# Optimization experiments

Measured on AMD Instinct MI355X. Metric: run time of the kernel, lower is better.

The kernel has to match this reference:

```python
import jax, jax.numpy as jnp
import numpy as np

B, N, DIM = 4, 4096, 1024
HEADS, DIM_HEAD, M = 16, 64, 128
DIM_INNER = HEADS * DIM_HEAD
SCALE = DIM_HEAD ** -0.5


def setup_inputs() -> dict:
    key = jax.random.key(0)
    ks = jax.random.split(key, 7)
    x = jax.random.normal(ks[0], (B, N, DIM), dtype=jnp.float32)
    mask = jax.random.bernoulli(ks[1], 0.9, (B, N))  # bool [b, n]
    W_qkv = jax.random.normal(ks[2], (DIM, 3 * DIM_INNER), dtype=jnp.float32) * (DIM ** -0.5)
    agent_tokens = jax.random.normal(ks[3], (HEADS, M, DIM_HEAD), dtype=jnp.float32) * 0.02
    W_qa = jax.random.normal(ks[4], (HEADS, HEADS), dtype=jnp.float32) * (HEADS ** -0.5)
    W_ak = jax.random.normal(ks[5], (HEADS, HEADS), dtype=jnp.float32) * (HEADS ** -0.5)
    W_out = jax.random.normal(ks[6], (DIM_INNER, DIM), dtype=jnp.float32) * (DIM_INNER ** -0.5)
    return {"x": x, "mask": mask, "W_qkv": W_qkv, "agent_tokens": agent_tokens,
            "W_qa": W_qa, "W_ak": W_ak, "W_out": W_out}


def reference(x, mask, W_qkv, agent_tokens, W_qa, W_ak, W_out):
    b, n, _ = x.shape
    h, m, d = agent_tokens.shape
    # qkv projection -> [3, b, h, n, d]  (layout matches 'b n (qkv h d)')
    qkv = (x @ W_qkv).reshape(b, n, 3, h, d).transpose(2, 0, 3, 1, 4)
    q, k, v = qkv[0], qkv[1], qkv[2]
    a = agent_tokens * SCALE  # [h, m, d]
    # stage 1: query-agent similarities [b, h, n, m]
    qa_sim = jnp.einsum('bhid,hjd->bhij', q, a)
    # stage 2: agent-key similarities [b, h, m, n]
    ak_sim = jnp.einsum('hid,bhjd->bhij', a, k)
    max_neg = -jnp.finfo(ak_sim.dtype).max
    ak_sim = jnp.where(mask[:, None, None, :], ak_sim, max_neg)
    qa_attn = jax.nn.softmax(qa_sim, axis=-1)
    ak_attn = jax.nn.softmax(ak_sim, axis=-1)
    # talking heads: 1x1 conv over head dim == head-mixing matmul
    qa_attn = jnp.einsum('gh,bhij->bgij', W_qa, qa_attn)
    ak_attn = jnp.einsum('gh,bhij->bgij', W_ak, ak_attn)
    agent_out = jnp.einsum('bhmn,bhnd->bhmd', ak_attn, v)    # [b, h, m, d]
    out = jnp.einsum('bhnm,bhmd->bhnd', qa_attn, agent_out)  # [b, h, n, d]
    out = jnp.where(mask[:, None, :, None], out, 0.0)
    out = out.transpose(0, 2, 1, 3).reshape(b, n, h * d)
    return out @ W_out
```

## Files before the change

kernel.cpp:

```cpp
#include <hip/hip_runtime.h>
#include <stdint.h>

#define DEVI __device__ __forceinline__

typedef __bf16 bf16x8 __attribute__((ext_vector_type(8)));
typedef float  f32x4  __attribute__((ext_vector_type(4)));
typedef unsigned int u32x2 __attribute__((ext_vector_type(2)));


DEVI unsigned short f2bf(float f) {
  union { float f; unsigned int u; } c; c.f = f;
  return (unsigned short)((c.u + 0x7fffu + ((c.u >> 16) & 1u)) >> 16);
}
DEVI float bf2f(unsigned short s) {
  union { unsigned int u; float f; } c; c.u = ((unsigned int)s) << 16;
  return c.f;
}
DEVI u32x2 pack4(float a, float b, float c, float d) {
  u32x2 r;
  r.x = (unsigned)f2bf(a) | ((unsigned)f2bf(b) << 16);
  r.y = (unsigned)f2bf(c) | ((unsigned)f2bf(d) << 16);
  return r;
}
DEVI bf16x8 ldg8(const unsigned short* p) { return *(const bf16x8*)p; }

DEVI void g2l16(const void* g, void* l) {
  __builtin_amdgcn_global_load_lds(
      (const __attribute__((address_space(1))) unsigned int*)g,
      (__attribute__((address_space(3))) unsigned int*)l, 16, 0, 0);
}

#define MFMA16(acc, a, b) acc = __builtin_amdgcn_mfma_f32_16x16x32_bf16((a), (b), (acc), 0, 0, 0)

#define VMCNT8() asm volatile("s_waitcnt vmcnt(8)")
#define VMCNT4() asm volatile("s_waitcnt vmcnt(4)")
#define VMCNT0() asm volatile("s_waitcnt vmcnt(0)")
#define LGKM0()  asm volatile("s_waitcnt lgkmcnt(0)")
#define SBAR()   __builtin_amdgcn_s_barrier()

__global__ __launch_bounds__(256) void k_prep(
    const float* __restrict__ x, const float* __restrict__ Wqkv,
    const float* __restrict__ ag, const float* __restrict__ Wout,
    unsigned short* __restrict__ Xb, unsigned short* __restrict__ WqkvT,
    unsigned short* __restrict__ Ab, unsigned short* __restrict__ WoT,
    float* __restrict__ rowsum)
{
  __shared__ float ldsT[32][33];
  const int tid = threadIdx.x;
  int bx = blockIdx.x;
  if (bx < 16384) {
    size_t i4 = ((size_t)bx * 256 + tid) * 4;
    f32x4 v = *(const f32x4*)&x[i4];
    *(u32x2*)&Xb[i4] = pack4(v[0], v[1], v[2], v[3]);
    return;
  }
  bx -= 16384;
  if (bx < 3072) {
    int jt = bx % 96, kt = bx / 96;
    int r32 = tid >> 3, c4 = (tid & 7) * 4;
    f32x4 v = *(const f32x4*)&Wqkv[(size_t)(kt * 32 + r32) * 3072 + jt * 32 + c4];
#pragma unroll
    for (int i = 0; i < 4; i++) ldsT[r32][c4 + i] = v[i];
    __syncthreads();
    float o0 = ldsT[c4 + 0][r32], o1 = ldsT[c4 + 1][r32];
    float o2 = ldsT[c4 + 2][r32], o3 = ldsT[c4 + 3][r32];
    *(u32x2*)&WqkvT[(size_t)(jt * 32 + r32) * 1024 + kt * 32 + c4] = pack4(o0, o1, o2, o3);
    return;
  }
  bx -= 3072;
  if (bx < 128) {
    size_t i4 = ((size_t)bx * 256 + tid) * 4;
    f32x4 v = *(const f32x4*)&ag[i4];
    *(u32x2*)&Ab[i4] = pack4(v[0] * 0.125f, v[1] * 0.125f, v[2] * 0.125f, v[3] * 0.125f);
    return;
  }
  bx -= 128;
  if (bx < 1024) {
    int ct = bx % 32, dt = bx / 32;
    int r32 = tid >> 3, c4 = (tid & 7) * 4;
    f32x4 v = *(const f32x4*)&Wout[(size_t)(dt * 32 + r32) * 1024 + ct * 32 + c4];
#pragma unroll
    for (int i = 0; i < 4; i++) ldsT[r32][c4 + i] = v[i];
    __syncthreads();
    float o0 = ldsT[c4 + 0][r32], o1 = ldsT[c4 + 1][r32];
    float o2 = ldsT[c4 + 2][r32], o3 = ldsT[c4 + 3][r32];
    *(u32x2*)&WoT[(size_t)(ct * 32 + r32) * 1024 + dt * 32 + c4] = pack4(o0, o1, o2, o3);
    return;
  }
  bx -= 1024;
  {
    const f32x4 z = {0.f, 0.f, 0.f, 0.f};
    *(f32x4*)&rowsum[((size_t)bx * 256 + tid) * 4] = z;
  }
}

DEVI void gemm_core_256(const unsigned short* __restrict__ A,
                        const unsigned short* __restrict__ Bt,
                        int row0, int col0, int swap,
                        unsigned short (*lds)[16384], f32x4 acc[8][4])
{
  const int tid = threadIdx.x, lane = tid & 63, w = tid >> 6;
  const int q = lane >> 4, r = lane & 15;
  const int wm = w >> 2, wn = w & 3;
  const int loff = r * 32 + ((q ^ ((r >> 1) & 3)) << 3);
  const int wslot = w * 512;
  const int scol = ((tid & 3) ^ ((tid >> 3) & 3)) << 3;
  const int srow = tid >> 2;
  const unsigned short* gA0 = A + (size_t)(row0 + srow) * 1024 + scol;
  const unsigned short* gA1 = gA0 + (size_t)128 * 1024;
  const unsigned short* gB0 = Bt + (size_t)(col0 + srow) * 1024 + scol;
  const unsigned short* gB1 = gB0 + (size_t)128 * 1024;
  const int aoff = (swap ? 8192 : 0) + wm * 4096;
  const int boff = (swap ? 0 : 8192) + wn * 2048;

  const f32x4 z = {0.f, 0.f, 0.f, 0.f};
#pragma unroll
  for (int i = 0; i < 8; i++)
#pragma unroll
    for (int j = 0; j < 4; j++) acc[i][j] = z;

#pragma unroll
  for (int pt = 0; pt < 3; ++pt) {
    unsigned short* lr = &lds[pt][0] + wslot;
    g2l16(gA0 + pt * 32, lr);
    g2l16(gA1 + pt * 32, lr + 4096);
    g2l16(gB0 + pt * 32, lr + 8192);
    g2l16(gB1 + pt * 32, lr + 12288);
  }
  VMCNT8();
  SBAR();

  for (int t = 0; t < 32; ++t) {
    const unsigned short* rp = &lds[t & 3][0];
    const unsigned short* pA = rp + aoff + loff;
    const unsigned short* pB = rp + boff + loff;
    bf16x8 af[4], bv[4];
#pragma unroll
    for (int rt = 0; rt < 4; rt++) af[rt] = *(const bf16x8*)(pA + rt * 512);
#pragma unroll
    for (int ct = 0; ct < 4; ct++) bv[ct] = *(const bf16x8*)(pB + ct * 512);
    if (t < 29) {
      unsigned short* lr = &lds[(t + 3) & 3][0] + wslot;
      size_t ko = (size_t)(t + 3) * 32;
      g2l16(gA0 + ko, lr);
      g2l16(gA1 + ko, lr + 4096);
    }
    SBAR();
    LGKM0();
    __builtin_amdgcn_s_setprio(1);
#pragma unroll
    for (int rt = 0; rt < 4; rt++)
#pragma unroll
      for (int ct = 0; ct < 4; ct++) MFMA16(acc[rt][ct], af[rt], bv[ct]);
    __builtin_amdgcn_s_setprio(0);
    SBAR();
#pragma unroll
    for (int rt = 0; rt < 4; rt++) af[rt] = *(const bf16x8*)(pA + (rt + 4) * 512);
    if (t < 29) {
      unsigned short* lr = &lds[(t + 3) & 3][0] + wslot;
      size_t ko = (size_t)(t + 3) * 32;
      g2l16(gB0 + ko, lr + 8192);
      g2l16(gB1 + ko, lr + 12288);
    }
    if (t < 29)      { VMCNT8(); }
    else if (t == 29) { VMCNT4(); }
    else if (t == 30) { VMCNT0(); }
    SBAR();
    LGKM0();
    __builtin_amdgcn_s_setprio(1);
#pragma unroll
    for (int rt = 0; rt < 4; rt++)
#pragma unroll
      for (int ct = 0; ct < 4; ct++) MFMA16(acc[rt + 4][ct], af[rt], bv[ct]);
    __builtin_amdgcn_s_setprio(0);
    SBAR();
  }
}

__global__ __launch_bounds__(512, 2) void k_gemm_qkv(
    const unsigned short* __restrict__ A, const unsigned short* __restrict__ Bt,
    unsigned short* __restrict__ Q, unsigned short* __restrict__ Kd,
    unsigned short* __restrict__ Vt)
{
  __shared__ __align__(16) unsigned short lds[4][16384];
  const int tid = threadIdx.x, lane = tid & 63, w = tid >> 6;
  const int q = lane >> 4, r = lane & 15, wm = w >> 2, wn = w & 3;
  const int row0 = blockIdx.x * 256, col0 = blockIdx.y * 256;
  const bool qk = blockIdx.y < 8;

  f32x4 acc[8][4];
  gemm_core_256(A, Bt, row0, col0, qk ? 1 : 0, lds, acc);

  const int b = row0 >> 12, row0b = row0 & 4095;
  if (qk) {
    unsigned short* dst = (col0 < 1024) ? Q : Kd;
    const int jb = (col0 & 1023) + wm * 128;
#pragma unroll
    for (int rt = 0; rt < 8; rt++)
#pragma unroll
      for (int ct = 0; ct < 4; ct++) {
        int j = jb + rt * 16 + 4 * q;
        int h = j >> 6, d0 = j & 63;
        int n = row0b + wn * 64 + ct * 16 + r;
        u32x2 pk = pack4(acc[rt][ct][0], acc[rt][ct][1], acc[rt][ct][2], acc[rt][ct][3]);
        *(u32x2*)&dst[(((size_t)(b * 16 + h)) * 4096 + n) * 64 + d0] = pk;
      }
  } else {
    const int jb = (col0 - 2048) + wn * 64;
#pragma unroll
    for (int rt = 0; rt < 8; rt++)
#pragma unroll
      for (int ct = 0; ct < 4; ct++) {
        int j = jb + ct * 16 + r;
        int h = j >> 6, d = j & 63;
        int n = row0b + wm * 128 + rt * 16 + 4 * q;
        u32x2 pk = pack4(acc[rt][ct][0], acc[rt][ct][1], acc[rt][ct][2], acc[rt][ct][3]);
        *(u32x2*)&Vt[(((size_t)(b * 16 + h)) * 64 + d) * 4096 + n] = pk;
      }
  }
}

__global__ __launch_bounds__(256, 2) void k_qk(
    const unsigned short* __restrict__ Q, const unsigned short* __restrict__ Kd,
    const unsigned short* __restrict__ Ab, const int* __restrict__ mask,
    unsigned short* __restrict__ QA, unsigned short* __restrict__ E,
    float* __restrict__ rowsum)
{
  const int tid = threadIdx.x, lane = tid & 63, w = tid >> 6;
  const int q = lane >> 4, r = lane & 15, wr = w >> 1, wc = w & 1;
  const int nt = blockIdx.x, h = blockIdx.y, b = blockIdx.z;
  const unsigned short* Qb = Q + (((size_t)(b * 16 + h)) * 4096 + nt * 128) * 64;
  const unsigned short* Kb = Kd + (((size_t)(b * 16 + h)) * 4096 + nt * 128) * 64;
  const unsigned short* Ah = Ab + (size_t)h * 8192;
  __shared__ float rs[2][128];
  const f32x4 z = {0.f, 0.f, 0.f, 0.f};

  {
    f32x4 acc[4][4];
#pragma unroll
    for (int i = 0; i < 4; i++)
#pragma unroll
      for (int j = 0; j < 4; j++) acc[i][j] = z;
#pragma unroll
    for (int ks = 0; ks < 2; ks++) {
      bf16x8 af[4], bv[4];
#pragma unroll
      for (int rt = 0; rt < 4; rt++) af[rt] = ldg8(Ah + (size_t)(64 * wr + 16 * rt + r) * 64 + ks * 32 + q * 8);
#pragma unroll
      for (int ct = 0; ct < 4; ct++) bv[ct] = ldg8(Qb + (size_t)(64 * wc + 16 * ct + r) * 64 + ks * 32 + q * 8);
#pragma unroll
      for (int rt = 0; rt < 4; rt++)
#pragma unroll
        for (int ct = 0; ct < 4; ct++) MFMA16(acc[rt][ct], af[rt], bv[ct]);
    }
    float cs[4];
#pragma unroll
    for (int ct = 0; ct < 4; ct++) {
      float s = 0.f;
#pragma unroll
      for (int rt = 0; rt < 4; rt++)
#pragma unroll
        for (int reg = 0; reg < 4; reg++) {
          float e = __expf(acc[rt][ct][reg]);
          acc[rt][ct][reg] = e; s += e;
        }
      s += __shfl_xor(s, 16); s += __shfl_xor(s, 32);
      cs[ct] = s;
    }
    if (q == 0) {
#pragma unroll
      for (int ct = 0; ct < 4; ct++) rs[wr][64 * wc + 16 * ct + r] = cs[ct];
    }
    __syncthreads();
#pragma unroll
    for (int ct = 0; ct < 4; ct++) {
      int nl = 64 * wc + 16 * ct + r;
      float inv = 1.0f / (rs[0][nl] + rs[1][nl]);
      int n = nt * 128 + nl;
      size_t base = (((size_t)(b * 16 + h)) * 4096 + n) * 128;
#pragma unroll
      for (int rt = 0; rt < 4; rt++) {
        int m0 = 64 * wr + 16 * rt + 4 * q;
        u32x2 pk = pack4(acc[rt][ct][0] * inv, acc[rt][ct][1] * inv,
                         acc[rt][ct][2] * inv, acc[rt][ct][3] * inv);
        *(u32x2*)&QA[base + m0] = pk;
      }
    }
  }
  __syncthreads();

  {
    f32x4 acc[4][4];
#pragma unroll
    for (int i = 0; i < 4; i++)
#pragma unroll
      for (int j = 0; j < 4; j++) acc[i][j] = z;
#pragma unroll
    for (int ks = 0; ks < 2; ks++) {
      bf16x8 af[4], bv[4];
#pragma unroll
      for (int rt = 0; rt < 4; rt++) af[rt] = ldg8(Kb + (size_t)(64 * wr + 16 * rt + r) * 64 + ks * 32 + q * 8);
#pragma unroll
      for (int ct = 0; ct < 4; ct++) bv[ct] = ldg8(Ah + (size_t)(64 * wc + 16 * ct + r) * 64 + ks * 32 + q * 8);
#pragma unroll
      for (int rt = 0; rt < 4; rt++)
#pragma unroll
        for (int ct = 0; ct < 4; ct++) MFMA16(acc[rt][ct], af[rt], bv[ct]);
    }
    float cs[4] = {0.f, 0.f, 0.f, 0.f};
#pragma unroll
    for (int rt = 0; rt < 4; rt++) {
      const int4 mkv = *(const int4*)&mask[b * 4096 + nt * 128 + 64 * wr + 16 * rt + 4 * q];
      int mka[4] = {mkv.x, mkv.y, mkv.z, mkv.w};
#pragma unroll
      for (int ct = 0; ct < 4; ct++) {
#pragma unroll
        for (int reg = 0; reg < 4; reg++) {
          float e = mka[reg] ? __expf(acc[rt][ct][reg]) : 0.0f;
          acc[rt][ct][reg] = e; cs[ct] += e;
        }
      }
    }
#pragma unroll
    for (int ct = 0; ct < 4; ct++) {
      float s = cs[ct];
      s += __shfl_xor(s, 16); s += __shfl_xor(s, 32);
      cs[ct] = s;
    }
    if (q == 0) {
#pragma unroll
      for (int ct = 0; ct < 4; ct++) rs[wr][64 * wc + 16 * ct + r] = cs[ct];
    }
#pragma unroll
    for (int ct = 0; ct < 4; ct++) {
      int m = 64 * wc + 16 * ct + r;
      size_t base = (((size_t)(b * 16 + h)) * 128 + m) * 4096;
#pragma unroll
      for (int rt = 0; rt < 4; rt++) {
        int n0 = nt * 128 + 64 * wr + 16 * rt + 4 * q;
        u32x2 pk = pack4(acc[rt][ct][0], acc[rt][ct][1], acc[rt][ct][2], acc[rt][ct][3]);
        *(u32x2*)&E[base + n0] = pk;
      }
    }
    __syncthreads();
    if (tid < 128) atomicAdd(&rowsum[(b * 16 + h) * 128 + tid], rs[0][tid] + rs[1][tid]);
  }
}

__global__ __launch_bounds__(256) void k_mix(
    const unsigned short* __restrict__ E, const float* __restrict__ rowsum,
    const float* __restrict__ Wak, unsigned short* __restrict__ MIX)
{
  const int tid = threadIdx.x;
  const int m = blockIdx.y, b = blockIdx.z;
  __shared__ float wv[256];
  __shared__ float inv[16];
  wv[tid] = Wak[tid];
  if (tid < 16) inv[tid] = 1.0f / rowsum[(b * 16 + tid) * 128 + m];
  __syncthreads();
  const int n0 = (blockIdx.x * 256 + tid) * 4;
  float p[16][4];
#pragma unroll
  for (int h = 0; h < 16; h++) {
    u32x2 v = *(const u32x2*)&E[(((size_t)(b * 16 + h)) * 128 + m) * 4096 + n0];
    float iv = inv[h];
    p[h][0] = bf2f((unsigned short)(v.x & 0xffff)) * iv;
    p[h][1] = bf2f((unsigned short)(v.x >> 16)) * iv;
    p[h][2] = bf2f((unsigned short)(v.y & 0xffff)) * iv;
    p[h][3] = bf2f((unsigned short)(v.y >> 16)) * iv;
  }
#pragma unroll
  for (int g = 0; g < 16; g++) {
    float s0 = 0.f, s1 = 0.f, s2 = 0.f, s3 = 0.f;
#pragma unroll
    for (int h = 0; h < 16; h++) {
      float wgh = wv[g * 16 + h];
      s0 += wgh * p[h][0]; s1 += wgh * p[h][1]; s2 += wgh * p[h][2]; s3 += wgh * p[h][3];
    }
    *(u32x2*)&MIX[(((size_t)(b * 16 + g)) * 128 + m) * 4096 + n0] = pack4(s0, s1, s2, s3);
  }
}

__global__ __launch_bounds__(256) void k_ao(
    const unsigned short* __restrict__ MIX, const unsigned short* __restrict__ Vt,
    float* __restrict__ P)
{
  const int tid = threadIdx.x, lane = tid & 63, w4 = tid >> 6;
  const int q = lane >> 4, r = lane & 15;
  const int kc = blockIdx.x, g = blockIdx.y, b = blockIdx.z;
  const unsigned short* Abase = MIX + ((size_t)(b * 16 + g)) * 128 * 4096;
  const unsigned short* Bbase = Vt + ((size_t)(b * 16 + g)) * 64 * 4096;
  f32x4 acc[2][4];
  const f32x4 z = {0.f, 0.f, 0.f, 0.f};
#pragma unroll
  for (int i = 0; i < 2; i++)
#pragma unroll
    for (int j = 0; j < 4; j++) acc[i][j] = z;
  for (int n = kc * 512; n < kc * 512 + 512; n += 32) {
    bf16x8 af[2], bv[4];
#pragma unroll
    for (int rt = 0; rt < 2; rt++) af[rt] = ldg8(Abase + (size_t)(32 * w4 + 16 * rt + r) * 4096 + n + q * 8);
#pragma unroll
    for (int ct = 0; ct < 4; ct++) bv[ct] = ldg8(Bbase + (size_t)(16 * ct + r) * 4096 + n + q * 8);
#pragma unroll
    for (int rt = 0; rt < 2; rt++)
#pragma unroll
      for (int ct = 0; ct < 4; ct++) MFMA16(acc[rt][ct], af[rt], bv[ct]);
  }
  float* Pp = P + (size_t)kc * 524288 + ((size_t)(b * 16 + g)) * 8192;
#pragma unroll
  for (int rt = 0; rt < 2; rt++)
#pragma unroll
    for (int ct = 0; ct < 4; ct++) {
      int m0 = 32 * w4 + 16 * rt + 4 * q, d = 16 * ct + r;
      *(f32x4*)&Pp[(size_t)d * 128 + m0] = acc[rt][ct];
    }
}

__global__ __launch_bounds__(256) void k_aored(
    const float* __restrict__ P, float* __restrict__ AOt)
{
  size_t i = ((size_t)blockIdx.x * 256 + threadIdx.x) * 4;
  f32x4 s = *(const f32x4*)&P[i];
#pragma unroll
  for (int kc = 1; kc < 8; kc++) {
    f32x4 v = *(const f32x4*)&P[(size_t)kc * 524288 + i];
    s[0] += v[0]; s[1] += v[1]; s[2] += v[2]; s[3] += v[3];
  }
  *(f32x4*)&AOt[i] = s;
}

__global__ __launch_bounds__(256) void k_mixqa(
    const unsigned short* __restrict__ QA, const float* __restrict__ Wqa,
    unsigned short* __restrict__ QAmix)
{
  const int tid = threadIdx.x;
  const int b = blockIdx.y;
  __shared__ float wv[256];
  wv[tid] = Wqa[tid];
  __syncthreads();
  const size_t i0 = ((size_t)blockIdx.x * 256 + tid) * 4;
  float p[16][4];
#pragma unroll
  for (int h = 0; h < 16; h++) {
    u32x2 v = *(const u32x2*)&QA[((size_t)(b * 16 + h)) * 524288 + i0];
    p[h][0] = bf2f((unsigned short)(v.x & 0xffff));
    p[h][1] = bf2f((unsigned short)(v.x >> 16));
    p[h][2] = bf2f((unsigned short)(v.y & 0xffff));
    p[h][3] = bf2f((unsigned short)(v.y >> 16));
  }
#pragma unroll
  for (int g = 0; g < 16; g++) {
    float s0 = 0.f, s1 = 0.f, s2 = 0.f, s3 = 0.f;
#pragma unroll
    for (int h = 0; h < 16; h++) {
      float wgh = wv[g * 16 + h];
      s0 += wgh * p[h][0]; s1 += wgh * p[h][1]; s2 += wgh * p[h][2]; s3 += wgh * p[h][3];
    }
    *(u32x2*)&QAmix[((size_t)(b * 16 + g)) * 524288 + i0] = pack4(s0, s1, s2, s3);
  }
}

__global__ __launch_bounds__(256) void k_o1(
    const unsigned short* __restrict__ QAmix, const float* __restrict__ AOt,
    unsigned short* __restrict__ out1)
{
  const int tid = threadIdx.x, lane = tid & 63, w4 = tid >> 6;
  const int q = lane >> 4, r = lane & 15;
  const int nt = blockIdx.x, g = blockIdx.y, b = blockIdx.z;
  const unsigned short* Bbase = QAmix + (((size_t)(b * 16 + g)) * 4096 + nt * 128) * 128;
  const float* Abase = AOt + ((size_t)(b * 16 + g)) * 8192;
  f32x4 acc[4][2];
  const f32x4 z = {0.f, 0.f, 0.f, 0.f};
#pragma unroll
  for (int i = 0; i < 4; i++)
#pragma unroll
    for (int j = 0; j < 2; j++) acc[i][j] = z;
#pragma unroll
  for (int ks = 0; ks < 4; ks++) {
    bf16x8 af[4], bv[2];
#pragma unroll
    for (int rt = 0; rt < 4; rt++) {
      const float* p = Abase + (size_t)(16 * rt + r) * 128 + ks * 32 + q * 8;
      f32x4 f0 = *(const f32x4*)p;
      f32x4 f1 = *(const f32x4*)(p + 4);
      bf16x8 t;
#pragma unroll
      for (int jj = 0; jj < 4; jj++) { t[jj] = (__bf16)f0[jj]; t[4 + jj] = (__bf16)f1[jj]; }
      af[rt] = t;
    }
#pragma unroll
    for (int ct = 0; ct < 2; ct++)
      bv[ct] = ldg8(Bbase + (size_t)(32 * w4 + 16 * ct + r) * 128 + ks * 32 + q * 8);
#pragma unroll
    for (int rt = 0; rt < 4; rt++)
#pragma unroll
      for (int ct = 0; ct < 2; ct++) MFMA16(acc[rt][ct], af[rt], bv[ct]);
  }
#pragma unroll
  for (int ct = 0; ct < 2; ct++) {
    int n = nt * 128 + 32 * w4 + 16 * ct + r;
    size_t base = ((size_t)b * 4096 + n) * 1024 + g * 64;
#pragma unroll
    for (int rt = 0; rt < 4; rt++) {
      int d0 = 16 * rt + 4 * q;
      u32x2 pk = pack4(acc[rt][ct][0], acc[rt][ct][1], acc[rt][ct][2], acc[rt][ct][3]);
      *(u32x2*)&out1[base + d0] = pk;
    }
  }
}

__global__ __launch_bounds__(512, 2) void k_fin2(
    const unsigned short* __restrict__ A, const unsigned short* __restrict__ Bt,
    const int* __restrict__ mask, float* __restrict__ out)
{
  __shared__ __align__(16) unsigned short lds[4][16384];
  const int tid = threadIdx.x, lane = tid & 63, w = tid >> 6;
  const int q = lane >> 4, r = lane & 15, wm = w >> 2, wn = w & 3;
  const int row0 = blockIdx.x * 256, col0 = blockIdx.y * 256;

  f32x4 acc[8][4];
  gemm_core_256(A, Bt, row0, col0, 0, lds, acc);

#pragma unroll
  for (int rt = 0; rt < 8; rt++) {
    const int4 mkv = *(const int4*)&mask[row0 + wm * 128 + rt * 16 + 4 * q];
    int mka[4] = {mkv.x, mkv.y, mkv.z, mkv.w};
#pragma unroll
    for (int reg = 0; reg < 4; reg++) {
      int row = row0 + wm * 128 + rt * 16 + 4 * q + reg;
#pragma unroll
      for (int ct = 0; ct < 4; ct++) {
        int c = col0 + wn * 64 + ct * 16 + r;
        out[(size_t)row * 1024 + c] = mka[reg] ? acc[rt][ct][reg] : 0.0f;
      }
    }
  }
}

extern "C" void kernel_launch(void* const* d_in, const int* in_sizes, int n_in,
                              void* d_out, int out_size, void* d_ws, size_t ws_size,
                              hipStream_t stream) {
  const float* x    = (const float*)d_in[0];
  const int*   mask = (const int*)d_in[1];
  const float* Wqkv = (const float*)d_in[2];
  const float* ag   = (const float*)d_in[3];
  const float* Wqa  = (const float*)d_in[4];
  const float* Wak  = (const float*)d_in[5];
  const float* Wout = (const float*)d_in[6];
  float* out = (float*)d_out;
  char* ws = (char*)d_ws;

  unsigned short* QA    = (unsigned short*)(ws + 0);
  unsigned short* QQ    = (unsigned short*)(ws + 67108864);
  unsigned short* KK    = (unsigned short*)(ws + 67108864 + 33554432);
  unsigned short* MIX   = QQ;
  unsigned short* out1  = QQ;
  unsigned short* VT    = (unsigned short*)(ws + 134217728);
  unsigned short* Xb    = (unsigned short*)(ws + 167772160);
  unsigned short* WqkvT = (unsigned short*)(ws + 167772160 + 33554432);
  unsigned short* E     = Xb;
  float*          Ppart = (float*)Xb;
  unsigned short* QAmix = Xb;
  char* sm = ws + 234881024;
  unsigned short* Ab  = (unsigned short*)(sm);
  unsigned short* WoT = (unsigned short*)(sm + 262144);
  float* rowsum = (float*)(sm + 262144 + 2097152);
  float* AOt    = (float*)(sm + 262144 + 2097152 + 32768);

  k_prep<<<20616, 256, 0, stream>>>(x, Wqkv, ag, Wout, Xb, WqkvT, Ab, WoT, rowsum);
  k_gemm_qkv<<<dim3(64, 12), 512, 0, stream>>>(Xb, WqkvT, QQ, KK, VT);
  k_qk<<<dim3(32, 16, 4), 256, 0, stream>>>(QQ, KK, Ab, mask, QA, E, rowsum);
  k_mix<<<dim3(4, 128, 4), 256, 0, stream>>>(E, rowsum, Wak, MIX);
  k_ao<<<dim3(8, 16, 4), 256, 0, stream>>>(MIX, VT, Ppart);
  k_aored<<<512, 256, 0, stream>>>(Ppart, AOt);
  k_mixqa<<<dim3(512, 4), 256, 0, stream>>>(QA, Wqa, QAmix);
  k_o1<<<dim3(32, 16, 4), 256, 0, stream>>>(QAmix, AOt, out1);
  k_fin2<<<dim3(64, 4), 512, 0, stream>>>(out1, WoT, mask, out);
}
```

Before: 468.0 us.

## Restructure shared GEMM core to K=64 double-buffered stages with 8-way swizzle

```diff
diff --git a/kernel.cpp b/kernel.cpp
--- a/kernel.cpp
+++ b/kernel.cpp
@@ -33,7 +33,6 @@
 #define MFMA16(acc, a, b) acc = __builtin_amdgcn_mfma_f32_16x16x32_bf16((a), (b), (acc), 0, 0, 0)
 
 #define VMCNT8() asm volatile("s_waitcnt vmcnt(8)")
-#define VMCNT4() asm volatile("s_waitcnt vmcnt(4)")
 #define VMCNT0() asm volatile("s_waitcnt vmcnt(0)")
 #define LGKM0()  asm volatile("s_waitcnt lgkmcnt(0)")
 #define SBAR()   __builtin_amdgcn_s_barrier()
@@ -97,21 +96,22 @@
 DEVI void gemm_core_256(const unsigned short* __restrict__ A,
                         const unsigned short* __restrict__ Bt,
                         int row0, int col0, int swap,
-                        unsigned short (*lds)[16384], f32x4 acc[8][4])
+                        unsigned short* ldsS, f32x4 acc[8][4])
 {
   const int tid = threadIdx.x, lane = tid & 63, w = tid >> 6;
   const int q = lane >> 4, r = lane & 15;
   const int wm = w >> 2, wn = w & 3;
-  const int loff = r * 32 + ((q ^ ((r >> 1) & 3)) << 3);
-  const int wslot = w * 512;
-  const int scol = ((tid & 3) ^ ((tid >> 3) & 3)) << 3;
-  const int srow = tid >> 2;
-  const unsigned short* gA0 = A + (size_t)(row0 + srow) * 1024 + scol;
-  const unsigned short* gA1 = gA0 + (size_t)128 * 1024;
-  const unsigned short* gB0 = Bt + (size_t)(col0 + srow) * 1024 + scol;
-  const unsigned short* gB1 = gB0 + (size_t)128 * 1024;
-  const int aoff = (swap ? 8192 : 0) + wm * 4096;
-  const int boff = (swap ? 0 : 8192) + wn * 2048;
+  const int abA = swap ? 2 : 0, abB = swap ? 0 : 2;
+  const int afhalf = wm, bvhalf = wn >> 1;
+  const int afr = r * 64;
+  const int bvr = ((wn & 1) * 64 + r) * 64;
+  const int cs0 = (q ^ (r & 7)) << 3;
+  const int cs1 = ((q + 4) ^ (r & 7)) << 3;
+  const int gr = tid >> 3;
+  const int gcol = ((tid & 7) ^ ((tid >> 3) & 7)) << 3;
+  const unsigned short* gA = A + (size_t)(row0 + gr) * 1024 + gcol;
+  const unsigned short* gB = Bt + (size_t)(col0 + gr) * 1024 + gcol;
+  const int ldst = w * 512;
 
   const f32x4 z = {0.f, 0.f, 0.f, 0.f};
 #pragma unroll
@@ -119,61 +119,106 @@
 #pragma unroll
     for (int j = 0; j < 4; j++) acc[i][j] = z;
 
-#pragma unroll
-  for (int pt = 0; pt < 3; ++pt) {
-    unsigned short* lr = &lds[pt][0] + wslot;
-    g2l16(gA0 + pt * 32, lr);
-    g2l16(gA1 + pt * 32, lr + 4096);
-    g2l16(gB0 + pt * 32, lr + 8192);
-    g2l16(gB1 + pt * 32, lr + 12288);
+  auto stageH = [&](const unsigned short* G, int half, int koff, int slot) {
+    const unsigned short* g0 = G + (size_t)half * 131072 + koff;
+    g2l16(g0, ldsS + slot + ldst);
+    g2l16(g0 + 65536, ldsS + slot + 4096 + ldst);
+  };
+
+#pragma unroll
+  for (int s = 0; s < 2; ++s) {
+    stageH(gB, 0, s * 64, ((s << 2) | 2 | 0) << 13);
+    stageH(gB, 1, s * 64, ((s << 2) | 2 | 1) << 13);
+    stageH(gA, 0, s * 64, ((s << 2) | 0 | 0) << 13);
+    stageH(gA, 1, s * 64, ((s << 2) | 0 | 1) << 13);
   }
   VMCNT8();
   SBAR();
 
-  for (int t = 0; t < 32; ++t) {
-    const unsigned short* rp = &lds[t & 3][0];
-    const unsigned short* pA = rp + aoff + loff;
-    const unsigned short* pB = rp + boff + loff;
-    bf16x8 af[4], bv[4];
-#pragma unroll
-    for (int rt = 0; rt < 4; rt++) af[rt] = *(const bf16x8*)(pA + rt * 512);
-#pragma unroll
-    for (int ct = 0; ct < 4; ct++) bv[ct] = *(const bf16x8*)(pB + ct * 512);
-    if (t < 29) {
-      unsigned short* lr = &lds[(t + 3) & 3][0] + wslot;
-      size_t ko = (size_t)(t + 3) * 32;
-      g2l16(gA0 + ko, lr);
-      g2l16(gA1 + ko, lr + 4096);
-    }
-    SBAR();
-    LGKM0();
+  auto kstep = [&](const int P, const int s) {
+    const int afb = (((P << 2) | abA | afhalf) << 13) + afr;
+    const int bvb = (((P << 2) | abB | bvhalf) << 13) + bvr;
+    bf16x8 af[4][2], bva[2][2], bvx[2][2];
+#pragma unroll
+    for (int rt = 0; rt < 4; rt++) {
+      af[rt][0] = *(const bf16x8*)&ldsS[afb + rt * 1024 + cs0];
+      af[rt][1] = *(const bf16x8*)&ldsS[afb + rt * 1024 + cs1];
+    }
+#pragma unroll
+    for (int ct = 0; ct < 2; ct++) {
+      bva[ct][0] = *(const bf16x8*)&ldsS[bvb + ct * 1024 + cs0];
+      bva[ct][1] = *(const bf16x8*)&ldsS[bvb + ct * 1024 + cs1];
+    }
+    SBAR(); LGKM0();
     __builtin_amdgcn_s_setprio(1);
 #pragma unroll
     for (int rt = 0; rt < 4; rt++)
 #pragma unroll
-      for (int ct = 0; ct < 4; ct++) MFMA16(acc[rt][ct], af[rt], bv[ct]);
+      for (int ct = 0; ct < 2; ct++) {
+        MFMA16(acc[rt][ct], af[rt][0], bva[ct][0]);
+        MFMA16(acc[rt][ct], af[rt][1], bva[ct][1]);
+      }
     __builtin_amdgcn_s_setprio(0);
     SBAR();
 #pragma unroll
-    for (int rt = 0; rt < 4; rt++) af[rt] = *(const bf16x8*)(pA + (rt + 4) * 512);
-    if (t < 29) {
-      unsigned short* lr = &lds[(t + 3) & 3][0] + wslot;
-      size_t ko = (size_t)(t + 3) * 32;
-      g2l16(gB0 + ko, lr + 8192);
-      g2l16(gB1 + ko, lr + 12288);
-    }
-    if (t < 29)      { VMCNT8(); }
-    else if (t == 29) { VMCNT4(); }
-    else if (t == 30) { VMCNT0(); }
-    SBAR();
-    LGKM0();
+    for (int ct = 0; ct < 2; ct++) {
+      bvx[ct][0] = *(const bf16x8*)&ldsS[bvb + (ct + 2) * 1024 + cs0];
+      bvx[ct][1] = *(const bf16x8*)&ldsS[bvb + (ct + 2) * 1024 + cs1];
+    }
+    SBAR(); LGKM0();
     __builtin_amdgcn_s_setprio(1);
 #pragma unroll
     for (int rt = 0; rt < 4; rt++)
 #pragma unroll
-      for (int ct = 0; ct < 4; ct++) MFMA16(acc[rt + 4][ct], af[rt], bv[ct]);
+      for (int ct = 0; ct < 2; ct++) {
+        MFMA16(acc[rt][ct + 2], af[rt][0], bvx[ct][0]);
+        MFMA16(acc[rt][ct + 2], af[rt][1], bvx[ct][1]);
+      }
     __builtin_amdgcn_s_setprio(0);
     SBAR();
+#pragma unroll
+    for (int rt = 0; rt < 4; rt++) {
+      af[rt][0] = *(const bf16x8*)&ldsS[afb + (rt + 4) * 1024 + cs0];
+      af[rt][1] = *(const bf16x8*)&ldsS[afb + (rt + 4) * 1024 + cs1];
+    }
+    if (s < 14) {
+      stageH(gB, 0, (s + 2) * 64, ((P << 2) | 2 | 0) << 13);
+      stageH(gB, 1, (s + 2) * 64, ((P << 2) | 2 | 1) << 13);
+    }
+    SBAR(); LGKM0();
+    __builtin_amdgcn_s_setprio(1);
+#pragma unroll
+    for (int rt = 0; rt < 4; rt++)
+#pragma unroll
+      for (int ct = 0; ct < 2; ct++) {
+        MFMA16(acc[rt + 4][ct], af[rt][0], bva[ct][0]);
+        MFMA16(acc[rt + 4][ct], af[rt][1], bva[ct][1]);
+      }
+    __builtin_amdgcn_s_setprio(0);
+    SBAR();
+    if (s < 14) {
+      stageH(gA, 0, (s + 2) * 64, ((P << 2) | 0 | 0) << 13);
+      stageH(gA, 1, (s + 2) * 64, ((P << 2) | 0 | 1) << 13);
+      VMCNT8();
+    } else if (s == 14) {
+      VMCNT0();
+    }
+    SBAR(); LGKM0();
+    __builtin_amdgcn_s_setprio(1);
+#pragma unroll
+    for (int rt = 0; rt < 4; rt++)
+#pragma unroll
+      for (int ct = 0; ct < 2; ct++) {
+        MFMA16(acc[rt + 4][ct + 2], af[rt][0], bvx[ct][0]);
+        MFMA16(acc[rt + 4][ct + 2], af[rt][1], bvx[ct][1]);
+      }
+    __builtin_amdgcn_s_setprio(0);
+    SBAR();
+  };
+
+  for (int it = 0; it < 8; ++it) {
+    kstep(0, 2 * it);
+    kstep(1, 2 * it + 1);
   }
 }
 
@@ -182,7 +227,7 @@
     unsigned short* __restrict__ Q, unsigned short* __restrict__ Kd,
     unsigned short* __restrict__ Vt)
 {
-  __shared__ __align__(16) unsigned short lds[4][16384];
+  __shared__ __align__(16) unsigned short lds[65536];
   const int tid = threadIdx.x, lane = tid & 63, w = tid >> 6;
   const int q = lane >> 4, r = lane & 15, wm = w >> 2, wn = w & 3;
   const int row0 = blockIdx.x * 256, col0 = blockIdx.y * 256;
@@ -514,7 +559,7 @@
     const unsigned short* __restrict__ A, const unsigned short* __restrict__ Bt,
     const int* __restrict__ mask, float* __restrict__ out)
 {
-  __shared__ __align__(16) unsigned short lds[4][16384];
+  __shared__ __align__(16) unsigned short lds[65536];
   const int tid = threadIdx.x, lane = tid & 63, w = tid >> 6;
   const int q = lane >> 4, r = lane & 15, wm = w >> 2, wn = w & 3;
   const int row0 = blockIdx.x * 256, col0 = blockIdx.y * 256;
```

After: 462.8 us. No clear change (-1.1%).
